# Performance work log

Hardware: AMD Instinct MI355X
Metric: run time of the kernel (lower is better)

Reference implementation:

```python
import jax, jax.numpy as jnp
import numpy as np

N_NODES = 50000
N_EDGES = 500000
N_GRAPHS = 256
D_IN, D_H1, D_H2, D_H3, D_OUT = 768, 256, 128, 64, 2


def _glorot(key, shape):
    fan_in, fan_out = shape[1], shape[0]
    lim = float(np.sqrt(6.0 / (fan_in + fan_out)))
    return jax.random.uniform(key, shape, jnp.float32, -lim, lim)


def setup_inputs() -> dict:
    key = jax.random.key(0)
    ks = jax.random.split(key, 12)
    x = jax.random.normal(ks[0], (N_NODES, D_IN), jnp.float32)
    edge_index = jax.random.randint(ks[1], (2, N_EDGES), 0, N_NODES, jnp.int64)
    batch = jnp.sort(jax.random.randint(ks[2], (N_NODES,), 0, N_GRAPHS, jnp.int64))
    return {
        "x": x,
        "edge_index": edge_index,
        "batch": batch,
        # SAGEConv1: out = lin_l(mean_aggr) + lin_r(x); bias only on lin_l (PyG default)
        "W1_l": _glorot(ks[3], (D_H1, D_IN)),
        "b1_l": jnp.zeros((D_H1,), jnp.float32),
        "W1_r": _glorot(ks[4], (D_H1, D_IN)),
        # SAGEConv2
        "W2_l": _glorot(ks[5], (D_H2, D_H1)),
        "b2_l": jnp.zeros((D_H2,), jnp.float32),
        "W2_r": _glorot(ks[6], (D_H2, D_H1)),
        # MLP head
        "W3": _glorot(ks[7], (D_H3, D_H2)),
        "b3": jnp.zeros((D_H3,), jnp.float32),
        "W4": _glorot(ks[8], (D_OUT, D_H3)),
        "b4": jnp.zeros((D_OUT,), jnp.float32),
    }


def _sage_conv(x, src, dst, deg_inv, W_l, b_l, W_r):
    # mean aggregation of neighbor features: scatter-add then divide by in-degree
    aggr = jax.ops.segment_sum(x[src], dst, num_segments=N_NODES)  # [N, d]
    aggr = aggr * deg_inv[:, None]
    return aggr @ W_l.T + b_l + x @ W_r.T


def reference(x, edge_index, batch, W1_l, b1_l, W1_r, W2_l, b2_l, W2_r, W3, b3, W4, b4):
    src, dst = edge_index[0], edge_index[1]
    deg = jax.ops.segment_sum(jnp.ones((N_EDGES,), x.dtype), dst, num_segments=N_NODES)
    deg_inv = jnp.where(deg > 0, 1.0 / jnp.maximum(deg, 1.0), 0.0)

    h = jax.nn.relu(_sage_conv(x, src, dst, deg_inv, W1_l, b1_l, W1_r))
    h = jax.nn.relu(_sage_conv(h, src, dst, deg_inv, W2_l, b2_l, W2_r))

    # global_mean_pool over graph ids
    pooled = jax.ops.segment_sum(h, batch, num_segments=N_GRAPHS)  # [G, 128]
    cnt = jax.ops.segment_sum(jnp.ones((N_NODES,), h.dtype), batch, num_segments=N_GRAPHS)
    pooled = pooled / jnp.maximum(cnt, 1.0)[:, None]

    # dropout is identity in eval mode
    h = pooled @ W3.T + b3
    h = h @ W4.T + b4
    return jax.nn.softmax(h, axis=-1)
```

## Files before the change

kernel.cpp:

```cpp
#include <hip/hip_runtime.h>
#include <cstdint>
#include <cstddef>

#define N_NODES 50000
#define N_EDGES 500000
#define N_GRAPHS 256
#define D_IN 768
#define D_H1 256
#define D_H2 128

typedef __attribute__((ext_vector_type(8))) __bf16 bf16x8;
typedef __attribute__((ext_vector_type(4))) float f32x4;

__device__ __forceinline__ float bf2f(uint32_t u) {
    union { uint32_t i; float f; } v; v.i = u << 16; return v.f;
}
__device__ __forceinline__ uint32_t f2bf(float f) {
    union { float f; uint32_t i; } v; v.f = f;
    uint32_t u = v.i;
    return (u + 0x7FFFu + ((u >> 16) & 1u)) >> 16;
}

__device__ __forceinline__ void pack_chunk(const float* __restrict__ src_row,
                                           uint16_t* __restrict__ out, int c) {
    float4 u = *(const float4*)src_row, v = *(const float4*)(src_row + 4);
    uint4 o;
    o.x = f2bf(u.x) | (f2bf(u.y) << 16);
    o.y = f2bf(u.z) | (f2bf(u.w) << 16);
    o.z = f2bf(v.x) | (f2bf(v.y) << 16);
    o.w = f2bf(v.z) | (f2bf(v.w) << 16);
    *(uint4*)(out + (size_t)c * 8) = o;
}

#define PA_BLK 18750
#define HI_BLK 1954
#define PW1_BLK 192
#define PW2_BLK 32
__global__ __launch_bounds__(256) void k_combo(
    const float* __restrict__ x, uint16_t* __restrict__ xp,
    const int* __restrict__ dst, int* __restrict__ deg,
    const float* __restrict__ W1l, const float* __restrict__ W1r, uint16_t* __restrict__ W1p,
    const float* __restrict__ W2l, const float* __restrict__ W2r, uint16_t* __restrict__ W2p)
{
    int b = blockIdx.x, tid = threadIdx.x;
    if (b < PA_BLK) {
        int c = b * 256 + tid;
        int l = c & 63, t = c >> 6;
        int kt = t % 24, mt = t / 24;
        int fr = l & 15, fq = l >> 4;
        pack_chunk(x + (size_t)(mt * 16 + fr) * 768 + kt * 32 + fq * 8, xp, c);
    } else if (b < PA_BLK + HI_BLK) {
        int e = (b - PA_BLK) * 256 + tid;
        if (e < N_EDGES) atomicAdd(&deg[dst[e]], 1);
    } else if (b < PA_BLK + HI_BLK + PW1_BLK) {
        int c = (b - PA_BLK - HI_BLK) * 256 + tid;
        int l = c & 63, t = c >> 6;
        int kt = t % 24, mt = t / 24;
        int fr = l & 15, fq = l >> 4;
        int row = mt * 16 + fr;
        const float* src = (row < 256) ? (W1l + (size_t)row * 768)
                                       : (W1r + (size_t)(row - 256) * 768);
        pack_chunk(src + kt * 32 + fq * 8, W1p, c);
    } else {
        int c = (b - PA_BLK - HI_BLK - PW1_BLK) * 256 + tid;
        int l = c & 63, t = c >> 6;
        int kt = t % 8, mt = t / 8;
        int fr = l & 15, fq = l >> 4;
        int row = mt * 16 + fr;
        const float* src = (row < 128) ? (W2l + (size_t)row * 256)
                                       : (W2r + (size_t)(row - 128) * 256);
        pack_chunk(src + kt * 32 + fq * 8, W2p, c);
    }
}

__global__ __launch_bounds__(256) void k_scan(
    const int* __restrict__ deg, unsigned long long* __restrict__ desc,
    int* __restrict__ row_start, float* __restrict__ deg_inv, int n)
{
    __shared__ int buf[256];
    __shared__ int s_prefix;
    int bid = blockIdx.x, t = threadIdx.x;
    int i = bid * 256 + t;
    int v = (i < n) ? deg[i] : 0;
    buf[t] = v; __syncthreads();
    for (int off = 1; off < 256; off <<= 1) {
        int u = (t >= off) ? buf[t - off] : 0;
        __syncthreads(); buf[t] += u; __syncthreads();
    }
    if (t == 0) {
        unsigned long long total = (unsigned long long)(unsigned)buf[255];
        __hip_atomic_store(&desc[bid], (1ull << 32) | total,
                           __ATOMIC_RELEASE, __HIP_MEMORY_SCOPE_AGENT);
        unsigned long long run = 0;
        for (int j = bid - 1; j >= 0; --j) {
            unsigned long long d;
            do {
                d = __hip_atomic_load(&desc[j], __ATOMIC_ACQUIRE, __HIP_MEMORY_SCOPE_AGENT);
            } while ((d >> 32) == 0);
            run += (d & 0xFFFFFFFFull);
            if ((d >> 32) == 2) break;
        }
        __hip_atomic_store(&desc[bid], (2ull << 32) | (run + total),
                           __ATOMIC_RELEASE, __HIP_MEMORY_SCOPE_AGENT);
        s_prefix = (int)run;
    }
    __syncthreads();
    int ex = s_prefix + buf[t] - v;
    if (i < n) {
        row_start[i] = ex;
        deg_inv[i] = (v > 0) ? (1.0f / (float)v) : 0.0f;
        if (i == n - 1) row_start[n] = ex + v;
    }
}

__global__ void k_fill(const int* __restrict__ src, const int* __restrict__ dst,
                       const int* __restrict__ row_start, int* __restrict__ cursor,
                       int* __restrict__ csr_src, int n) {
    int e = blockIdx.x * blockDim.x + threadIdx.x;
    if (e < n) {
        int d = dst[e];
        int pos = row_start[d] + atomicAdd(&cursor[d], 1);
        csr_src[pos] = src[e];
    }
}

__global__ __launch_bounds__(256, 2) void k_mgemm(
    const uint16_t* __restrict__ Ap, const uint16_t* __restrict__ Bp,
    uint16_t* __restrict__ C, int M, int N, int KT)
{
    const int tid = threadIdx.x;
    const int wave = tid >> 6, lane = tid & 63;
    const int fr = lane & 15, fq = lane >> 4;
    const int bn = blockIdx.x * 256, bm = blockIdx.y * 128;
    const int wm = (wave >> 1) * 64, wn = (wave & 1) * 128;
    const int mtiles = (M + 15) >> 4;

    const bf16x8* ap[4];
    const bf16x8* bp[8];
    #pragma unroll
    for (int mi = 0; mi < 4; ++mi) {
        int mt = ((bm + wm) >> 4) + mi;
        if (mt > mtiles - 1) mt = mtiles - 1;
        ap[mi] = (const bf16x8*)Ap + (size_t)mt * KT * 64 + lane;
    }
    #pragma unroll
    for (int ni = 0; ni < 8; ++ni) {
        int nt = ((bn + wn) >> 4) + ni;
        bp[ni] = (const bf16x8*)Bp + (size_t)nt * KT * 64 + lane;
    }

    f32x4 acc[4][8] = {};
    bf16x8 a0[4], b0[8], a1[4], b1[8];

    auto lA = [&](int kt, bf16x8* d) {
        #pragma unroll
        for (int mi = 0; mi < 4; ++mi) d[mi] = ap[mi][kt * 64];
    };
    auto lB = [&](int kt, bf16x8* d) {
        #pragma unroll
        for (int ni = 0; ni < 8; ++ni) d[ni] = bp[ni][kt * 64];
    };
    auto step = [&](bf16x8* a, bf16x8* b) {
        #pragma unroll
        for (int mi = 0; mi < 4; ++mi)
            #pragma unroll
            for (int ni = 0; ni < 8; ++ni)
                acc[mi][ni] = __builtin_amdgcn_mfma_f32_16x16x32_bf16(
                    a[mi], b[ni], acc[mi][ni], 0, 0, 0);
    };

    lA(0, a0); lB(0, b0);
    for (int ks = 0; ks < KT; ks += 2) {
        lA(ks + 1, a1); lB(ks + 1, b1);
        step(a0, b0);
        if (ks + 2 < KT) { lA(ks + 2, a0); lB(ks + 2, b0); }
        step(a1, b1);
    }

    #pragma unroll
    for (int mi = 0; mi < 4; ++mi) {
        #pragma unroll
        for (int r = 0; r < 4; ++r) {
            int row = bm + wm + mi * 16 + fq * 4 + r;
            if (row >= M) continue;
            #pragma unroll
            for (int ni = 0; ni < 8; ++ni) {
                int col = bn + wn + ni * 16 + fr;
                C[(size_t)row * N + col] = (uint16_t)f2bf(acc[mi][ni][r]);
            }
        }
    }
}

__global__ __launch_bounds__(256) void k_agg1(
    const uint16_t* __restrict__ y, const int* __restrict__ row_start,
    const int* __restrict__ csr, const float* __restrict__ deg_inv,
    const float* __restrict__ bias, uint16_t* __restrict__ h1p)
{
    int node = blockIdx.x * 8 + (threadIdx.x >> 5);
    if (node >= N_NODES) return;
    int c = threadIdx.x & 31;
    int s = row_start[node], e = row_start[node + 1];
    float a[8] = {};
    int p = s;
    for (; p + 1 < e; p += 2) {
        uint4 t0 = *(const uint4*)(y + (size_t)csr[p] * 512 + c * 8);
        uint4 t1 = *(const uint4*)(y + (size_t)csr[p + 1] * 512 + c * 8);
        a[0] += bf2f(t0.x & 0xFFFF) + bf2f(t1.x & 0xFFFF);
        a[1] += bf2f(t0.x >> 16)    + bf2f(t1.x >> 16);
        a[2] += bf2f(t0.y & 0xFFFF) + bf2f(t1.y & 0xFFFF);
        a[3] += bf2f(t0.y >> 16)    + bf2f(t1.y >> 16);
        a[4] += bf2f(t0.z & 0xFFFF) + bf2f(t1.z & 0xFFFF);
        a[5] += bf2f(t0.z >> 16)    + bf2f(t1.z >> 16);
        a[6] += bf2f(t0.w & 0xFFFF) + bf2f(t1.w & 0xFFFF);
        a[7] += bf2f(t0.w >> 16)    + bf2f(t1.w >> 16);
    }
    if (p < e) {
        uint4 t0 = *(const uint4*)(y + (size_t)csr[p] * 512 + c * 8);
        a[0] += bf2f(t0.x & 0xFFFF); a[1] += bf2f(t0.x >> 16);
        a[2] += bf2f(t0.y & 0xFFFF); a[3] += bf2f(t0.y >> 16);
        a[4] += bf2f(t0.z & 0xFFFF); a[5] += bf2f(t0.z >> 16);
        a[6] += bf2f(t0.w & 0xFFFF); a[7] += bf2f(t0.w >> 16);
    }
    float w = deg_inv[node];
    uint4 tx = *(const uint4*)(y + (size_t)node * 512 + 256 + c * 8);
    float4 b0 = *(const float4*)(bias + c * 8);
    float4 b1 = *(const float4*)(bias + c * 8 + 4);
    float v0 = fmaxf(a[0] * w + bf2f(tx.x & 0xFFFF) + b0.x, 0.f);
    float v1 = fmaxf(a[1] * w + bf2f(tx.x >> 16)    + b0.y, 0.f);
    float v2 = fmaxf(a[2] * w + bf2f(tx.y & 0xFFFF) + b0.z, 0.f);
    float v3 = fmaxf(a[3] * w + bf2f(tx.y >> 16)    + b0.w, 0.f);
    float v4 = fmaxf(a[4] * w + bf2f(tx.z & 0xFFFF) + b1.x, 0.f);
    float v5 = fmaxf(a[5] * w + bf2f(tx.z >> 16)    + b1.y, 0.f);
    float v6 = fmaxf(a[6] * w + bf2f(tx.w & 0xFFFF) + b1.z, 0.f);
    float v7 = fmaxf(a[7] * w + bf2f(tx.w >> 16)    + b1.w, 0.f);
    uint4 o;
    o.x = f2bf(v0) | (f2bf(v1) << 16);
    o.y = f2bf(v2) | (f2bf(v3) << 16);
    o.z = f2bf(v4) | (f2bf(v5) << 16);
    o.w = f2bf(v6) | (f2bf(v7) << 16);
    uint32_t addr = (((node >> 4) * 8 + (c >> 2)) * 64 + (c & 3) * 16 + (node & 15));
    *(uint4*)(h1p + (size_t)addr * 8) = o;
}

__global__ __launch_bounds__(256) void k_agg2pool(
    const uint16_t* __restrict__ y, const int* __restrict__ row_start,
    const int* __restrict__ csr, const float* __restrict__ deg_inv,
    const float* __restrict__ bias, const int* __restrict__ batch,
    float* __restrict__ pooled)
{
    int node = blockIdx.x * 4 + (threadIdx.x >> 6);
    if (node >= N_NODES) return;
    int lane = threadIdx.x & 63;
    int s = row_start[node], e = row_start[node + 1];
    float a0 = 0.f, a1 = 0.f;
    int p = s;
    for (; p + 1 < e; p += 2) {
        uint32_t t0 = *(const uint32_t*)(y + (size_t)csr[p] * 256 + lane * 2);
        uint32_t t1 = *(const uint32_t*)(y + (size_t)csr[p + 1] * 256 + lane * 2);
        a0 += bf2f(t0 & 0xFFFF) + bf2f(t1 & 0xFFFF);
        a1 += bf2f(t0 >> 16)    + bf2f(t1 >> 16);
    }
    if (p < e) {
        uint32_t t0 = *(const uint32_t*)(y + (size_t)csr[p] * 256 + lane * 2);
        a0 += bf2f(t0 & 0xFFFF);
        a1 += bf2f(t0 >> 16);
    }
    float w = deg_inv[node];
    uint32_t tx = *(const uint32_t*)(y + (size_t)node * 256 + 128 + lane * 2);
    float2 b = *(const float2*)(bias + lane * 2);
    float h0 = fmaxf(a0 * w + bf2f(tx & 0xFFFF) + b.x, 0.f);
    float h1 = fmaxf(a1 * w + bf2f(tx >> 16)    + b.y, 0.f);
    int g = batch[node];
    atomicAdd(&pooled[g * 128 + lane * 2], h0);
    atomicAdd(&pooled[g * 128 + lane * 2 + 1], h1);
}

__global__ void k_head(const float* __restrict__ pooled, const int* __restrict__ batch,
                       const float* __restrict__ W3, const float* __restrict__ b3,
                       const float* __restrict__ W4, const float* __restrict__ b4,
                       float* __restrict__ out)
{
    int g = blockIdx.x;
    int j = threadIdx.x;
    __shared__ float p[128];
    __shared__ float hid[64];
    __shared__ float logit[2];
    __shared__ float s_inv;
    if (j == 0) {
        int lo = 0, hi = N_NODES;
        while (lo < hi) { int m = (lo + hi) >> 1; if (batch[m] < g) lo = m + 1; else hi = m; }
        int lo2 = lo, hi2 = N_NODES;
        while (lo2 < hi2) { int m = (lo2 + hi2) >> 1; if (batch[m] < g + 1) lo2 = m + 1; else hi2 = m; }
        int cnt = lo2 - lo;
        s_inv = 1.0f / (float)(cnt > 0 ? cnt : 1);
    }
    __syncthreads();
    p[j]      = pooled[g * 128 + j] * s_inv;
    p[j + 64] = pooled[g * 128 + 64 + j] * s_inv;
    __syncthreads();
    float s = b3[j];
    #pragma unroll 4
    for (int k = 0; k < 128; ++k) s = fmaf(p[k], W3[j * 128 + k], s);
    hid[j] = s;
    __syncthreads();
    if (j < 2) {
        float l = b4[j];
        for (int k = 0; k < 64; ++k) l = fmaf(hid[k], W4[j * 64 + k], l);
        logit[j] = l;
    }
    __syncthreads();
    if (j == 0) {
        float m = fmaxf(logit[0], logit[1]);
        float e0 = expf(logit[0] - m), e1 = expf(logit[1] - m);
        float inv = 1.0f / (e0 + e1);
        out[g * 2 + 0] = e0 * inv;
        out[g * 2 + 1] = e1 * inv;
    }
}

extern "C" void kernel_launch(void* const* d_in, const int* in_sizes, int n_in,
                              void* d_out, int out_size, void* d_ws, size_t ws_size,
                              hipStream_t stream)
{
    const float* x     = (const float*)d_in[0];
    const int*   ei    = (const int*)d_in[1];
    const int*   batch = (const int*)d_in[2];
    const float* W1l   = (const float*)d_in[3];
    const float* b1l   = (const float*)d_in[4];
    const float* W1r   = (const float*)d_in[5];
    const float* W2l   = (const float*)d_in[6];
    const float* b2l   = (const float*)d_in[7];
    const float* W2r   = (const float*)d_in[8];
    const float* W3    = (const float*)d_in[9];
    const float* b3    = (const float*)d_in[10];
    const float* W4    = (const float*)d_in[11];
    const float* b4    = (const float*)d_in[12];
    float* out = (float*)d_out;

    const int* e_src = ei;
    const int* e_dst = ei + N_EDGES;

    char* ws = (char*)d_ws;
    size_t off = 0;
    auto alloc = [&](size_t bytes) -> void* {
        void* p = ws + off;
        off = (off + bytes + 255) & ~(size_t)255;
        return p;
    };
    int*      deg       = (int*)alloc((size_t)N_NODES * 4);
    int*      cursor    = (int*)alloc((size_t)N_NODES * 4);
    float*    pooled    = (float*)alloc((size_t)N_GRAPHS * D_H2 * 4);
    unsigned long long* desc = (unsigned long long*)alloc(196 * 8);
    size_t zero_span = off;
    int*      row_start = (int*)alloc((size_t)(N_NODES + 1) * 4);
    int*      csr_src   = (int*)alloc((size_t)N_EDGES * 4);
    float*    deg_inv   = (float*)alloc((size_t)N_NODES * 4);
    uint16_t* W1p       = (uint16_t*)alloc((size_t)512 * 768 * 2);
    uint16_t* W2p       = (uint16_t*)alloc((size_t)256 * 256 * 2);
    uint16_t* xp        = (uint16_t*)alloc((size_t)N_NODES * D_IN * 2);
    uint16_t* y1        = (uint16_t*)alloc((size_t)N_NODES * 512 * 2);
    uint16_t* h1p       = (uint16_t*)alloc((size_t)N_NODES * 256 * 2);

    uint16_t* y2 = xp;

    hipMemsetAsync(deg, 0, zero_span, stream);

    k_combo<<<PA_BLK + HI_BLK + PW1_BLK + PW2_BLK, 256, 0, stream>>>(
        x, xp, e_dst, deg, W1l, W1r, W1p, W2l, W2r, W2p);
    k_scan<<<196, 256, 0, stream>>>(deg, desc, row_start, deg_inv, N_NODES);
    k_fill<<<(N_EDGES + 255) / 256, 256, 0, stream>>>(e_src, e_dst, row_start, cursor, csr_src, N_EDGES);
    dim3 g1(2, (N_NODES + 127) / 128);
    k_mgemm<<<g1, 256, 0, stream>>>(xp, W1p, y1, N_NODES, 512, 24);
    k_agg1<<<(N_NODES + 7) / 8, 256, 0, stream>>>(y1, row_start, csr_src, deg_inv, b1l, h1p);
    dim3 g2(1, (N_NODES + 127) / 128);
    k_mgemm<<<g2, 256, 0, stream>>>(h1p, W2p, y2, N_NODES, 256, 8);
    k_agg2pool<<<(N_NODES + 3) / 4, 256, 0, stream>>>(y2, row_start, csr_src, deg_inv, b2l, batch, pooled);
    k_head<<<N_GRAPHS, 64, 0, stream>>>(pooled, batch, W3, b3, W4, b4, out);
}
```

Measured before the change: 531.3 us.

## Fuse CSR scan and fill into first GEMM launch to overlap graph build

```diff
diff --git a/kernel.cpp b/kernel.cpp
--- a/kernel.cpp
+++ b/kernel.cpp
@@ -8,6 +8,10 @@
 #define D_IN 768
 #define D_H1 256
 #define D_H2 128
+
+#define CSR_BLK 98
+#define NSCAN 196
+#define FILL_THREADS (NSCAN * 256)
 
 typedef __attribute__((ext_vector_type(8))) __bf16 bf16x8;
 typedef __attribute__((ext_vector_type(4))) float f32x4;
@@ -73,65 +77,69 @@
     }
 }
 
-__global__ __launch_bounds__(256) void k_scan(
+__global__ __launch_bounds__(256, 2) void k_gemm_csr(
+    const uint16_t* __restrict__ Ap, const uint16_t* __restrict__ Bp,
+    uint16_t* __restrict__ C, int M, int N, int KT,
     const int* __restrict__ deg, unsigned long long* __restrict__ desc,
-    int* __restrict__ row_start, float* __restrict__ deg_inv, int n)
+    int* __restrict__ row_start, float* __restrict__ deg_inv,
+    const int* __restrict__ e_src, const int* __restrict__ e_dst,
+    int* __restrict__ cursor, int* __restrict__ csr_src, int* __restrict__ scan_done)
 {
     __shared__ int buf[256];
     __shared__ int s_prefix;
-    int bid = blockIdx.x, t = threadIdx.x;
-    int i = bid * 256 + t;
-    int v = (i < n) ? deg[i] : 0;
-    buf[t] = v; __syncthreads();
-    for (int off = 1; off < 256; off <<= 1) {
-        int u = (t >= off) ? buf[t - off] : 0;
-        __syncthreads(); buf[t] += u; __syncthreads();
-    }
-    if (t == 0) {
-        unsigned long long total = (unsigned long long)(unsigned)buf[255];
-        __hip_atomic_store(&desc[bid], (1ull << 32) | total,
-                           __ATOMIC_RELEASE, __HIP_MEMORY_SCOPE_AGENT);
-        unsigned long long run = 0;
-        for (int j = bid - 1; j >= 0; --j) {
-            unsigned long long d;
-            do {
-                d = __hip_atomic_load(&desc[j], __ATOMIC_ACQUIRE, __HIP_MEMORY_SCOPE_AGENT);
-            } while ((d >> 32) == 0);
-            run += (d & 0xFFFFFFFFull);
-            if ((d >> 32) == 2) break;
-        }
-        __hip_atomic_store(&desc[bid], (2ull << 32) | (run + total),
-                           __ATOMIC_RELEASE, __HIP_MEMORY_SCOPE_AGENT);
-        s_prefix = (int)run;
-    }
-    __syncthreads();
-    int ex = s_prefix + buf[t] - v;
-    if (i < n) {
-        row_start[i] = ex;
-        deg_inv[i] = (v > 0) ? (1.0f / (float)v) : 0.0f;
-        if (i == n - 1) row_start[n] = ex + v;
-    }
-}
-
-__global__ void k_fill(const int* __restrict__ src, const int* __restrict__ dst,
-                       const int* __restrict__ row_start, int* __restrict__ cursor,
-                       int* __restrict__ csr_src, int n) {
-    int e = blockIdx.x * blockDim.x + threadIdx.x;
-    if (e < n) {
-        int d = dst[e];
-        int pos = row_start[d] + atomicAdd(&cursor[d], 1);
-        csr_src[pos] = src[e];
-    }
-}
-
-__global__ __launch_bounds__(256, 2) void k_mgemm(
-    const uint16_t* __restrict__ Ap, const uint16_t* __restrict__ Bp,
-    uint16_t* __restrict__ C, int M, int N, int KT)
-{
     const int tid = threadIdx.x;
+
+    if (blockIdx.y < CSR_BLK) {
+        int cid = blockIdx.y * 2 + blockIdx.x;
+        int i = cid * 256 + tid;
+        int v = (i < N_NODES) ? deg[i] : 0;
+        buf[tid] = v; __syncthreads();
+        for (int off = 1; off < 256; off <<= 1) {
+            int u = (tid >= off) ? buf[tid - off] : 0;
+            __syncthreads(); buf[tid] += u; __syncthreads();
+        }
+        if (tid == 0) {
+            unsigned long long total = (unsigned long long)(unsigned)buf[255];
+            __hip_atomic_store(&desc[cid], (1ull << 32) | total,
+                               __ATOMIC_RELEASE, __HIP_MEMORY_SCOPE_AGENT);
+            unsigned long long run = 0;
+            for (int j = cid - 1; j >= 0; --j) {
+                unsigned long long d;
+                do {
+                    d = __hip_atomic_load(&desc[j], __ATOMIC_ACQUIRE, __HIP_MEMORY_SCOPE_AGENT);
+                } while ((d >> 32) == 0);
+                run += (d & 0xFFFFFFFFull);
+                if ((d >> 32) == 2) break;
+            }
+            __hip_atomic_store(&desc[cid], (2ull << 32) | (run + total),
+                               __ATOMIC_RELEASE, __HIP_MEMORY_SCOPE_AGENT);
+            s_prefix = (int)run;
+        }
+        __syncthreads();
+        int ex = s_prefix + buf[tid] - v;
+        if (i < N_NODES) {
+            row_start[i] = ex;
+            deg_inv[i] = (v > 0) ? (1.0f / (float)v) : 0.0f;
+            if (i == N_NODES - 1) row_start[N_NODES] = ex + v;
+        }
+        __syncthreads();
+        if (tid == 0) {
+            __hip_atomic_fetch_add(scan_done, 1, __ATOMIC_ACQ_REL, __HIP_MEMORY_SCOPE_AGENT);
+            while (__hip_atomic_load(scan_done, __ATOMIC_ACQUIRE, __HIP_MEMORY_SCOPE_AGENT) < NSCAN)
+                __builtin_amdgcn_s_sleep(1);
+        }
+        __syncthreads();
+        for (int e = cid * 256 + tid; e < N_EDGES; e += FILL_THREADS) {
+            int d = e_dst[e];
+            int pos = row_start[d] + atomicAdd(&cursor[d], 1);
+            csr_src[pos] = e_src[e];
+        }
+        return;
+    }
+
     const int wave = tid >> 6, lane = tid & 63;
     const int fr = lane & 15, fq = lane >> 4;
-    const int bn = blockIdx.x * 256, bm = blockIdx.y * 128;
+    const int bn = blockIdx.x * 256, bm = (blockIdx.y - CSR_BLK) * 128;
     const int wm = (wave >> 1) * 64, wn = (wave & 1) * 128;
     const int mtiles = (M + 15) >> 4;
 
@@ -192,6 +200,74 @@
     }
 }
 
+__global__ __launch_bounds__(256, 2) void k_mgemm(
+    const uint16_t* __restrict__ Ap, const uint16_t* __restrict__ Bp,
+    uint16_t* __restrict__ C, int M, int N, int KT)
+{
+    const int tid = threadIdx.x;
+    const int wave = tid >> 6, lane = tid & 63;
+    const int fr = lane & 15, fq = lane >> 4;
+    const int bn = blockIdx.x * 256, bm = blockIdx.y * 128;
+    const int wm = (wave >> 1) * 64, wn = (wave & 1) * 128;
+    const int mtiles = (M + 15) >> 4;
+
+    const bf16x8* ap[4];
+    const bf16x8* bp[8];
+    #pragma unroll
+    for (int mi = 0; mi < 4; ++mi) {
+        int mt = ((bm + wm) >> 4) + mi;
+        if (mt > mtiles - 1) mt = mtiles - 1;
+        ap[mi] = (const bf16x8*)Ap + (size_t)mt * KT * 64 + lane;
+    }
+    #pragma unroll
+    for (int ni = 0; ni < 8; ++ni) {
+        int nt = ((bn + wn) >> 4) + ni;
+        bp[ni] = (const bf16x8*)Bp + (size_t)nt * KT * 64 + lane;
+    }
+
+    f32x4 acc[4][8] = {};
+    bf16x8 a0[4], b0[8], a1[4], b1[8];
+
+    auto lA = [&](int kt, bf16x8* d) {
+        #pragma unroll
+        for (int mi = 0; mi < 4; ++mi) d[mi] = ap[mi][kt * 64];
+    };
+    auto lB = [&](int kt, bf16x8* d) {
+        #pragma unroll
+        for (int ni = 0; ni < 8; ++ni) d[ni] = bp[ni][kt * 64];
+    };
+    auto step = [&](bf16x8* a, bf16x8* b) {
+        #pragma unroll
+        for (int mi = 0; mi < 4; ++mi)
+            #pragma unroll
+            for (int ni = 0; ni < 8; ++ni)
+                acc[mi][ni] = __builtin_amdgcn_mfma_f32_16x16x32_bf16(
+                    a[mi], b[ni], acc[mi][ni], 0, 0, 0);
+    };
+
+    lA(0, a0); lB(0, b0);
+    for (int ks = 0; ks < KT; ks += 2) {
+        lA(ks + 1, a1); lB(ks + 1, b1);
+        step(a0, b0);
+        if (ks + 2 < KT) { lA(ks + 2, a0); lB(ks + 2, b0); }
+        step(a1, b1);
+    }
+
+    #pragma unroll
+    for (int mi = 0; mi < 4; ++mi) {
+        #pragma unroll
+        for (int r = 0; r < 4; ++r) {
+            int row = bm + wm + mi * 16 + fq * 4 + r;
+            if (row >= M) continue;
+            #pragma unroll
+            for (int ni = 0; ni < 8; ++ni) {
+                int col = bn + wn + ni * 16 + fr;
+                C[(size_t)row * N + col] = (uint16_t)f2bf(acc[mi][ni][r]);
+            }
+        }
+    }
+}
+
 __global__ __launch_bounds__(256) void k_agg1(
     const uint16_t* __restrict__ y, const int* __restrict__ row_start,
     const int* __restrict__ csr, const float* __restrict__ deg_inv,
@@ -203,19 +279,21 @@
     int s = row_start[node], e = row_start[node + 1];
     float a[8] = {};
     int p = s;
-    for (; p + 1 < e; p += 2) {
+    for (; p + 3 < e; p += 4) {
         uint4 t0 = *(const uint4*)(y + (size_t)csr[p] * 512 + c * 8);
         uint4 t1 = *(const uint4*)(y + (size_t)csr[p + 1] * 512 + c * 8);
-        a[0] += bf2f(t0.x & 0xFFFF) + bf2f(t1.x & 0xFFFF);
-        a[1] += bf2f(t0.x >> 16)    + bf2f(t1.x >> 16);
-        a[2] += bf2f(t0.y & 0xFFFF) + bf2f(t1.y & 0xFFFF);
-        a[3] += bf2f(t0.y >> 16)    + bf2f(t1.y >> 16);
-        a[4] += bf2f(t0.z & 0xFFFF) + bf2f(t1.z & 0xFFFF);
-        a[5] += bf2f(t0.z >> 16)    + bf2f(t1.z >> 16);
-        a[6] += bf2f(t0.w & 0xFFFF) + bf2f(t1.w & 0xFFFF);
-        a[7] += bf2f(t0.w >> 16)    + bf2f(t1.w >> 16);
-    }
-    if (p < e) {
+        uint4 t2 = *(const uint4*)(y + (size_t)csr[p + 2] * 512 + c * 8);
+        uint4 t3 = *(const uint4*)(y + (size_t)csr[p + 3] * 512 + c * 8);
+        a[0] += (bf2f(t0.x & 0xFFFF) + bf2f(t1.x & 0xFFFF)) + (bf2f(t2.x & 0xFFFF) + bf2f(t3.x & 0xFFFF));
+        a[1] += (bf2f(t0.x >> 16)    + bf2f(t1.x >> 16))    + (bf2f(t2.x >> 16)    + bf2f(t3.x >> 16));
+        a[2] += (bf2f(t0.y & 0xFFFF) + bf2f(t1.y & 0xFFFF)) + (bf2f(t2.y & 0xFFFF) + bf2f(t3.y & 0xFFFF));
+        a[3] += (bf2f(t0.y >> 16)    + bf2f(t1.y >> 16))    + (bf2f(t2.y >> 16)    + bf2f(t3.y >> 16));
+        a[4] += (bf2f(t0.z & 0xFFFF) + bf2f(t1.z & 0xFFFF)) + (bf2f(t2.z & 0xFFFF) + bf2f(t3.z & 0xFFFF));
+        a[5] += (bf2f(t0.z >> 16)    + bf2f(t1.z >> 16))    + (bf2f(t2.z >> 16)    + bf2f(t3.z >> 16));
+        a[6] += (bf2f(t0.w & 0xFFFF) + bf2f(t1.w & 0xFFFF)) + (bf2f(t2.w & 0xFFFF) + bf2f(t3.w & 0xFFFF));
+        a[7] += (bf2f(t0.w >> 16)    + bf2f(t1.w >> 16))    + (bf2f(t2.w >> 16)    + bf2f(t3.w >> 16));
+    }
+    for (; p < e; ++p) {
         uint4 t0 = *(const uint4*)(y + (size_t)csr[p] * 512 + c * 8);
         a[0] += bf2f(t0.x & 0xFFFF); a[1] += bf2f(t0.x >> 16);
         a[2] += bf2f(t0.y & 0xFFFF); a[3] += bf2f(t0.y >> 16);
@@ -255,13 +333,15 @@
     int s = row_start[node], e = row_start[node + 1];
     float a0 = 0.f, a1 = 0.f;
     int p = s;
-    for (; p + 1 < e; p += 2) {
+    for (; p + 3 < e; p += 4) {
         uint32_t t0 = *(const uint32_t*)(y + (size_t)csr[p] * 256 + lane * 2);
         uint32_t t1 = *(const uint32_t*)(y + (size_t)csr[p + 1] * 256 + lane * 2);
-        a0 += bf2f(t0 & 0xFFFF) + bf2f(t1 & 0xFFFF);
-        a1 += bf2f(t0 >> 16)    + bf2f(t1 >> 16);
-    }
-    if (p < e) {
+        uint32_t t2 = *(const uint32_t*)(y + (size_t)csr[p + 2] * 256 + lane * 2);
+        uint32_t t3 = *(const uint32_t*)(y + (size_t)csr[p + 3] * 256 + lane * 2);
+        a0 += (bf2f(t0 & 0xFFFF) + bf2f(t1 & 0xFFFF)) + (bf2f(t2 & 0xFFFF) + bf2f(t3 & 0xFFFF));
+        a1 += (bf2f(t0 >> 16)    + bf2f(t1 >> 16))    + (bf2f(t2 >> 16)    + bf2f(t3 >> 16));
+    }
+    for (; p < e; ++p) {
         uint32_t t0 = *(const uint32_t*)(y + (size_t)csr[p] * 256 + lane * 2);
         a0 += bf2f(t0 & 0xFFFF);
         a1 += bf2f(t0 >> 16);
@@ -351,7 +431,8 @@
     int*      deg       = (int*)alloc((size_t)N_NODES * 4);
     int*      cursor    = (int*)alloc((size_t)N_NODES * 4);
     float*    pooled    = (float*)alloc((size_t)N_GRAPHS * D_H2 * 4);
-    unsigned long long* desc = (unsigned long long*)alloc(196 * 8);
+    unsigned long long* desc = (unsigned long long*)alloc(NSCAN * 8);
+    int*      scan_done = (int*)alloc(4);
     size_t zero_span = off;
     int*      row_start = (int*)alloc((size_t)(N_NODES + 1) * 4);
     int*      csr_src   = (int*)alloc((size_t)N_EDGES * 4);
@@ -368,10 +449,10 @@
 
     k_combo<<<PA_BLK + HI_BLK + PW1_BLK + PW2_BLK, 256, 0, stream>>>(
         x, xp, e_dst, deg, W1l, W1r, W1p, W2l, W2r, W2p);
-    k_scan<<<196, 256, 0, stream>>>(deg, desc, row_start, deg_inv, N_NODES);
-    k_fill<<<(N_EDGES + 255) / 256, 256, 0, stream>>>(e_src, e_dst, row_start, cursor, csr_src, N_EDGES);
-    dim3 g1(2, (N_NODES + 127) / 128);
-    k_mgemm<<<g1, 256, 0, stream>>>(xp, W1p, y1, N_NODES, 512, 24);
+    dim3 g1(2, CSR_BLK + (N_NODES + 127) / 128);
+    k_gemm_csr<<<g1, 256, 0, stream>>>(xp, W1p, y1, N_NODES, 512, 24,
+                                       deg, desc, row_start, deg_inv,
+                                       e_src, e_dst, cursor, csr_src, scan_done);
     k_agg1<<<(N_NODES + 7) / 8, 256, 0, stream>>>(y1, row_start, csr_src, deg_inv, b1l, h1p);
     dim3 g2(1, (N_NODES + 127) / 128);
     k_mgemm<<<g2, 256, 0, stream>>>(h1p, W2p, y2, N_NODES, 256, 8);
```

After: 541.8 us. No clear change (+2.0%).
